# Kernel tuning notes

Measured on AMD Instinct MI355X. Metric: run time of the kernel, lower is better.

The kernel has to match this reference:

```python
import jax, jax.numpy as jnp
import numpy as np

D_MODEL = 2048
N_HEADS = 32
N_KV = 8
HEAD_DIM = D_MODEL // N_HEADS  # 64
D_FF = 8192
ROPE_BASE = 10000.0
EPS = 1e-5
B, S = 2, 2048


def setup_inputs() -> dict:
    key = jax.random.key(0)
    ks = jax.random.split(key, 8)
    s = 0.02
    qkv_out = (N_HEADS + 2 * N_KV) * HEAD_DIM
    return {
        "x": jax.random.normal(ks[0], (B, S, D_MODEL), jnp.float32),
        "w_norm1": jnp.ones((D_MODEL,), jnp.float32),
        "w_qkv": jax.random.normal(ks[1], (D_MODEL, qkv_out), jnp.float32) * s,
        "w_out": jax.random.normal(ks[2], (D_MODEL, D_MODEL), jnp.float32) * s,
        "w_norm2": jnp.ones((D_MODEL,), jnp.float32),
        "w_gate": jax.random.normal(ks[3], (D_MODEL, D_FF), jnp.float32) * s,
        "w_up": jax.random.normal(ks[4], (D_MODEL, D_FF), jnp.float32) * s,
        "w_down": jax.random.normal(ks[5], (D_FF, D_MODEL), jnp.float32) * s,
    }


def _rmsnorm(x, w):
    var = jnp.mean(x * x, axis=-1, keepdims=True)
    return x * jax.lax.rsqrt(var + EPS) * w


def _rope(x, cos, sin):
    # x: [b, s, h, d]; cos/sin: [s, d/2]; non-interleaved (NeoX half split)
    half = x.shape[-1] // 2
    x1, x2 = x[..., :half], x[..., half:]
    c = cos[None, :, None, :]
    sn = sin[None, :, None, :]
    return jnp.concatenate([x1 * c - x2 * sn, x1 * sn + x2 * c], axis=-1)


def _forward(x, w_norm1, w_qkv, w_out, w_norm2, w_gate, w_up, w_down):
    b, s, d = x.shape
    # --- attention block ---
    h = _rmsnorm(x, w_norm1)
    qkv = h @ w_qkv  # [b, s, (H + 2*KV) * hd]
    q = qkv[..., : N_HEADS * HEAD_DIM].reshape(b, s, N_HEADS, HEAD_DIM)
    kv = qkv[..., N_HEADS * HEAD_DIM:].reshape(b, s, 2, N_KV, HEAD_DIM)
    k, v = kv[:, :, 0], kv[:, :, 1]

    inv_freq = 1.0 / (ROPE_BASE ** (jnp.arange(0, HEAD_DIM, 2, dtype=jnp.float32) / HEAD_DIM))
    t = jnp.arange(s, dtype=jnp.float32)
    freqs = t[:, None] * inv_freq[None, :]  # [s, hd/2]
    cos, sin = jnp.cos(freqs), jnp.sin(freqs)
    q = _rope(q, cos, sin)
    k = _rope(k, cos, sin)

    # GQA: repeat_interleave kv heads to match q heads
    g = N_HEADS // N_KV
    k = jnp.repeat(k, g, axis=2)  # [b, s, H, hd]
    v = jnp.repeat(v, g, axis=2)

    scale = 1.0 / np.sqrt(HEAD_DIM)
    scores = jnp.einsum("bqhd,bkhd->bhqk", q, k) * scale
    causal = jnp.tril(jnp.ones((s, s), bool))
    scores = jnp.where(causal[None, None], scores, jnp.finfo(scores.dtype).min)
    attn = jax.nn.softmax(scores, axis=-1)
    ctx = jnp.einsum("bhqk,bkhd->bqhd", attn, v).reshape(b, s, N_HEADS * HEAD_DIM)
    x = x + ctx @ w_out

    # --- MLP block (SwiGLU) ---
    h2 = _rmsnorm(x, w_norm2)
    mlp = (jax.nn.silu(h2 @ w_gate) * (h2 @ w_up)) @ w_down
    return x + mlp


def reference(x, w_norm1, w_qkv, w_out, w_norm2, w_gate, w_up, w_down):
    return _forward(x, w_norm1, w_qkv, w_out, w_norm2, w_gate, w_up, w_down)
```

## Files before the change

kernel.cpp:

```cpp
#include <hip/hip_runtime.h>
#include <stdint.h>

#define D_MODEL 2048
#define S_LEN   2048
#define NTOK    4096
#define QKV_N   3072
#define DFF     8192

typedef float  f32x4   __attribute__((ext_vector_type(4)));
typedef float  f32x16  __attribute__((ext_vector_type(16)));
typedef __bf16 bf16x8  __attribute__((ext_vector_type(8)));
typedef unsigned short u16;
typedef unsigned short u16x8 __attribute__((ext_vector_type(8)));

__device__ __forceinline__ float b2f(u16 u){ union{float f; uint32_t i;} v; v.i = ((uint32_t)u) << 16; return v.f; }
__device__ __forceinline__ u16 f2b(float f){
  union{float f; uint32_t i;} v; v.f = f;
  uint32_t r = v.i + 0x7FFFu + ((v.i >> 16) & 1u);
  return (u16)(r >> 16);
}

__device__ __forceinline__ void gload_lds16(const void* gsrc, void* ldst){
  __builtin_amdgcn_global_load_lds(
      (const __attribute__((address_space(1))) void*)gsrc,
      (__attribute__((address_space(3))) void*)ldst,
      16, 0, 0);
}

__device__ __forceinline__ void conv_tiles(const float* W, u16* WT,
    int Nfull, int Kt, int Nt, int k0g, int n0g, void* ldsbuf)
{
  if (W == nullptr) return;
  float* tf = (float*)ldsbuf;
  const int tt  = threadIdx.x;
  const int nTn = Nt >> 6;
  const int nT  = (Kt >> 6) * nTn;
  const int bid = (blockIdx.z * gridDim.y + blockIdx.y) * gridDim.x + blockIdx.x;
  const int gsz = gridDim.x * gridDim.y * gridDim.z;
  const int c4 = (tt & 15) << 2;
  const int r  = tt >> 4;
  for (int tile = bid; tile < nT; tile += gsz) {
    const int k0 = (tile / nTn) << 6, n0 = (tile % nTn) << 6;
    __syncthreads();
    if (tt < 256) {
#pragma unroll
      for (int i = 0; i < 4; ++i) {
        int row = r + i * 16;
        float4 v = *reinterpret_cast<const float4*>(&W[(size_t)(k0g + k0 + row) * Nfull + n0g + n0 + c4]);
        tf[row * 65 + c4 + 0] = v.x; tf[row * 65 + c4 + 1] = v.y;
        tf[row * 65 + c4 + 2] = v.z; tf[row * 65 + c4 + 3] = v.w;
      }
    }
    __syncthreads();
    if (tt < 256) {
#pragma unroll
      for (int i = 0; i < 4; ++i) {
        int n = r + i * 16;
        ushort4 ov;
        ov.x = f2b(tf[(c4 + 0) * 65 + n]); ov.y = f2b(tf[(c4 + 1) * 65 + n]);
        ov.z = f2b(tf[(c4 + 2) * 65 + n]); ov.w = f2b(tf[(c4 + 3) * 65 + n]);
        *reinterpret_cast<ushort4*>(&WT[(size_t)(n0 + n) * Kt + k0 + c4]) = ov;
      }
    }
  }
}

__global__ __launch_bounds__(256) void wconv_kernel(const float* __restrict__ W, u16* __restrict__ WT,
                                                    int Nfull, int Kt, int Nt, int k0g, int n0g)
{
  __shared__ float tile[64 * 65];
  conv_tiles(W, WT, Nfull, Kt, Nt, k0g, n0g, tile);
}

__global__ void sincos_kernel(float* __restrict__ ct, float* __restrict__ st)
{
  int idx = blockIdx.x * 256 + threadIdx.x;
  if (idx >= S_LEN * 32) return;
  int p = idx >> 5, i = idx & 31;
  double freq = pow(10000.0, -((double)(2*i)) / 64.0);
  double ang  = (double)p * freq;
  ct[idx] = (float)cos(ang);
  st[idx] = (float)sin(ang);
}

template<bool BF16IN>
__global__ __launch_bounds__(256) void rmsnorm_kernel(const void* __restrict__ xin, const float* __restrict__ w, u16* __restrict__ out,
                                                      float* __restrict__ xout,
                                                      const float* cvW, u16* cvWT, int cvNfull, int cvKt, int cvNt, int cvK0g, int cvN0g)
{
  __shared__ float tfbuf[64 * 65];
  const int row = blockIdx.x;
  const int t = threadIdx.x;
  float v[8];
  if (BF16IN) {
    const u16* xr = ((const u16*)xin) + (size_t)row * D_MODEL;
    u16x8 a = *reinterpret_cast<const u16x8*>(&xr[t*8]);
#pragma unroll
    for (int j = 0; j < 8; ++j) v[j] = b2f(a[j]);
  } else {
    const float* xr = ((const float*)xin) + (size_t)row * D_MODEL;
    float4 a = *reinterpret_cast<const float4*>(&xr[t*8]);
    float4 c = *reinterpret_cast<const float4*>(&xr[t*8+4]);
    v[0]=a.x; v[1]=a.y; v[2]=a.z; v[3]=a.w; v[4]=c.x; v[5]=c.y; v[6]=c.z; v[7]=c.w;
  }
  if (xout) {
    float4 o0 = {v[0], v[1], v[2], v[3]};
    float4 o1 = {v[4], v[5], v[6], v[7]};
    *reinterpret_cast<float4*>(&xout[(size_t)row * D_MODEL + t*8])     = o0;
    *reinterpret_cast<float4*>(&xout[(size_t)row * D_MODEL + t*8 + 4]) = o1;
  }
  float ss = 0.f;
#pragma unroll
  for (int j = 0; j < 8; ++j) ss += v[j]*v[j];
#pragma unroll
  for (int d = 1; d < 64; d <<= 1) ss += __shfl_xor(ss, d);
  __shared__ float red[4];
  if ((t & 63) == 0) red[t >> 6] = ss;
  __syncthreads();
  ss = red[0] + red[1] + red[2] + red[3];
  const float sc = rsqrtf(ss * (1.0f / (float)D_MODEL) + 1e-5f);
  float4 w0 = *reinterpret_cast<const float4*>(&w[t*8]);
  float4 w1 = *reinterpret_cast<const float4*>(&w[t*8+4]);
  u16x8 o;
  o[0]=f2b(v[0]*sc*w0.x); o[1]=f2b(v[1]*sc*w0.y); o[2]=f2b(v[2]*sc*w0.z); o[3]=f2b(v[3]*sc*w0.w);
  o[4]=f2b(v[4]*sc*w1.x); o[5]=f2b(v[5]*sc*w1.y); o[6]=f2b(v[6]*sc*w1.z); o[7]=f2b(v[7]*sc*w1.w);
  *reinterpret_cast<u16x8*>(&out[(size_t)row * D_MODEL + t*8]) = o;
  conv_tiles(cvW, cvWT, cvNfull, cvKt, cvNt, cvK0g, cvN0g, tfbuf);
}

template<int EPI>
__device__ __forceinline__ void epi_store(size_t idx, float v, float* Cf, u16* Cb,
                                          const float* resf, const u16* resb, const u16* other)
{
  if (EPI == 2)      Cb[idx] = f2b(v / (1.0f + __expf(-v)));
  else if (EPI == 3) Cb[idx] = f2b(v * b2f(other[idx]));
  else if (EPI == 4) Cb[idx] = f2b(v);
  else if (EPI == 5) Cf[idx] += v;
  else if (EPI == 6) Cb[idx] = f2b(v + resf[idx]);
  else if (EPI == 7) Cf[idx] = v + b2f(resb[idx]);
  else if (EPI == 8) { if (blockIdx.z == 0) Cf[idx] += v; else Cb[idx] = f2b(v); }
}

template<int EPI>
__global__ __launch_bounds__(512, 2) void gemm8p_kernel(
    const u16* __restrict__ A, const u16* __restrict__ BT,
    int K, int lda, int ldb, int ldc, int n_off, int kstep,
    float* Cf, u16* Cb,
    const float* __restrict__ resf, const u16* __restrict__ resb, const u16* other,
    const float* cvW, u16* cvWT, int cvNfull, int cvKt, int cvNt, int cvK0g, int cvN0g)
{
  __shared__ u16 lds[65536];
  const int tid = threadIdx.x;
  const int w = tid >> 6, lane = tid & 63;
  const int g = lane >> 4, lr = lane & 15;
  const int wm = w >> 2, wn = w & 3;
  const int bn = blockIdx.x, bm = blockIdx.y;
  const int koff = blockIdx.z * kstep;
  const int NT = K >> 6;
  const int NI = NT >> 1;

  const int srow = tid >> 3;
  const int sg   = (tid & 7) ^ (srow & 7);
  const u16* Asrc = A  + (size_t)(bm * 256) * lda + koff;
  const u16* Bsrc = BT + (size_t)(bn * 256) * ldb + koff;

  const int agc0 = ((0 + g) ^ (lr & 7)) * 8;
  const int agc1 = ((4 + g) ^ (lr & 7)) * 8;

  f32x4 acc[8][4];
#pragma unroll
  for (int i = 0; i < 8; ++i)
#pragma unroll
    for (int j = 0; j < 4; ++j) acc[i][j] = (f32x4){0.f, 0.f, 0.f, 0.f};
  bf16x8 af[4][2], bf0[2][2], bf1[2][2];

#define STAGE_H(isB, h, b, T) do {                                           \
    int tc = ((T) < NT) ? (T) : (NT - 1);                                    \
    const u16* sb = (isB) ? Bsrc : Asrc;                                     \
    const int  sld = (isB) ? ldb : lda;                                      \
    const u16* s0 = sb + (size_t)((h)*128 + srow) * sld + tc*64 + sg*8;      \
    u16* dst = &lds[(b)*32768 + (isB)*16384 + (h)*8192 + tid*8];             \
    gload_lds16(s0, dst);                                                    \
    gload_lds16(s0 + (size_t)64 * sld, dst + 4096);                          \
  } while (0)

#define LOADA(mih, b) { _Pragma("unroll") for (int q = 0; q < 4; ++q) {      \
    const u16* rp = &lds[(b)*32768 + (wm*128 + (mih)*64 + q*16 + lr) * 64];  \
    af[q][0] = *(const bf16x8*)(rp + agc0);                                  \
    af[q][1] = *(const bf16x8*)(rp + agc1); } }

#define LOADB(dst, nih, b) { _Pragma("unroll") for (int nq = 0; nq < 2; ++nq) { \
    const u16* rp = &lds[(b)*32768 + 16384 + (wn*64 + (nih)*32 + nq*16 + lr) * 64]; \
    dst[nq][0] = *(const bf16x8*)(rp + agc0);                                \
    dst[nq][1] = *(const bf16x8*)(rp + agc1); } }

#define MM(mih, nih, BF) {                                                   \
    __builtin_amdgcn_s_setprio(1);                                           \
    _Pragma("unroll") for (int kk = 0; kk < 2; ++kk)                         \
      _Pragma("unroll") for (int q = 0; q < 4; ++q)                          \
        _Pragma("unroll") for (int nq = 0; nq < 2; ++nq)                     \
          acc[(mih)*4+q][(nih)*2+nq] = __builtin_amdgcn_mfma_f32_16x16x32_bf16( \
              af[q][kk], BF[nq][kk], acc[(mih)*4+q][(nih)*2+nq], 0, 0, 0);   \
    __builtin_amdgcn_s_setprio(0); }

#define SYNC_MID  __builtin_amdgcn_s_barrier();                              \
                  asm volatile("s_waitcnt lgkmcnt(0)" ::: "memory");         \
                  __builtin_amdgcn_sched_barrier(0);
#define PHEND     __builtin_amdgcn_s_barrier();
#define PHEND_VM  asm volatile("s_waitcnt vmcnt(4)" ::: "memory");           \
                  __builtin_amdgcn_s_barrier();

  STAGE_H(0, 0, 0, 0); STAGE_H(0, 1, 0, 0);
  STAGE_H(1, 0, 0, 0); STAGE_H(1, 1, 0, 0);
  STAGE_H(1, 0, 1, 1); STAGE_H(1, 1, 1, 1);
  asm volatile("s_waitcnt vmcnt(4)" ::: "memory");
  __builtin_amdgcn_s_barrier();

  for (int i = 0; i < NI; ++i) {
    const int t0 = 2 * i;
    LOADA(0, 0); LOADB(bf0, 0, 0);
    STAGE_H(0, 0, 1, t0 + 1);
    SYNC_MID; MM(0, 0, bf0); PHEND;
    LOADB(bf1, 1, 0);
    STAGE_H(0, 1, 1, t0 + 1);
    SYNC_MID; MM(0, 1, bf1); PHEND;
    LOADA(1, 0);
    STAGE_H(1, 0, 0, t0 + 2);
    SYNC_MID; MM(1, 1, bf1); PHEND;
    STAGE_H(1, 1, 0, t0 + 2);
    SYNC_MID; MM(1, 0, bf0); PHEND_VM;
    LOADA(0, 1); LOADB(bf0, 0, 1);
    STAGE_H(0, 0, 0, t0 + 2);
    SYNC_MID; MM(0, 0, bf0); PHEND;
    LOADB(bf1, 1, 1);
    STAGE_H(0, 1, 0, t0 + 2);
    SYNC_MID; MM(0, 1, bf1); PHEND;
    LOADA(1, 1);
    STAGE_H(1, 0, 1, t0 + 3);
    SYNC_MID; MM(1, 1, bf1); PHEND;
    STAGE_H(1, 1, 1, t0 + 3);
    SYNC_MID; MM(1, 0, bf0); PHEND_VM;
  }
#undef STAGE_H
#undef LOADA
#undef LOADB
#undef MM

#pragma unroll
  for (int mi = 0; mi < 8; ++mi) {
    const int rowOff = (mi >> 2) * 64 + (mi & 3) * 16;
#pragma unroll
    for (int ni = 0; ni < 4; ++ni) {
      const int colOff = (ni >> 1) * 32 + (ni & 1) * 16;
#pragma unroll
      for (int j = 0; j < 4; ++j) {
        int row = bm*256 + wm*128 + rowOff + g*4 + j;
        int col = n_off + bn*256 + wn*64 + colOff + lr;
        epi_store<EPI>((size_t)row * ldc + col, acc[mi][ni][j], Cf, Cb, resf, resb, other);
      }
    }
  }
  conv_tiles(cvW, cvWT, cvNfull, cvKt, cvNt, cvK0g, cvN0g, lds);
}

template<int EPI>
__global__ __launch_bounds__(512) void gemm128_kernel(
    const u16* __restrict__ A, const u16* __restrict__ BT,
    int K, int lda, int ldb, int ldc, int n_off,
    float* Cf, u16* Cb,
    const float* __restrict__ resf, const u16* __restrict__ resb, const u16* other,
    const float* cvW, u16* cvWT, int cvNfull, int cvKt, int cvNt, int cvK0g, int cvN0g)
{
  __shared__ u16 lds[49152];
  const int tid = threadIdx.x;
  const int w = tid >> 6, lane = tid & 63;
  const int g = lane >> 4, lr = lane & 15;
  const int wm = w >> 2, wn = w & 3;
  const int bn = blockIdx.x, bm = blockIdx.y;
  const int NT = K >> 6;
  const int NI = NT >> 1;

  const int srow = tid >> 3;
  const int sg   = (tid & 7) ^ (srow & 7);
  const u16* Asrc = A  + (size_t)(bm * 128) * lda;
  const u16* Bsrc = BT + (size_t)(bn * 256) * ldb;

  const int agc0 = ((0 + g) ^ (lr & 7)) * 8;
  const int agc1 = ((4 + g) ^ (lr & 7)) * 8;

  f32x4 acc[4][4];
#pragma unroll
  for (int i = 0; i < 4; ++i)
#pragma unroll
    for (int j = 0; j < 4; ++j) acc[i][j] = (f32x4){0.f, 0.f, 0.f, 0.f};
  bf16x8 af[2][2], bf0[2][2], bf1[2][2];

#define STAGE_A(b, T) do {                                                   \
    int tc = ((T) < NT) ? (T) : (NT - 1);                                    \
    const u16* s0 = Asrc + (size_t)srow * lda + tc*64 + sg*8;                \
    u16* dst = &lds[(b)*24576 + tid*8];                                      \
    gload_lds16(s0, dst);                                                    \
    gload_lds16(s0 + (size_t)64 * lda, dst + 4096);                          \
  } while (0)

#define STAGE_BH(h, b, T) do {                                               \
    int tc = ((T) < NT) ? (T) : (NT - 1);                                    \
    const u16* s0 = Bsrc + (size_t)((h)*128 + srow) * ldb + tc*64 + sg*8;    \
    u16* dst = &lds[(b)*24576 + 8192 + (h)*8192 + tid*8];                    \
    gload_lds16(s0, dst);                                                    \
    gload_lds16(s0 + (size_t)64 * ldb, dst + 4096);                         \
  } while (0)

#define LOADA(mih, b) { _Pragma("unroll") for (int q = 0; q < 2; ++q) {      \
    const u16* rp = &lds[(b)*24576 + (wm*64 + (mih)*32 + q*16 + lr) * 64];   \
    af[q][0] = *(const bf16x8*)(rp + agc0);                                  \
    af[q][1] = *(const bf16x8*)(rp + agc1); } }

#define LOADB(dst, nih, b) { _Pragma("unroll") for (int nq = 0; nq < 2; ++nq) { \
    const u16* rp = &lds[(b)*24576 + 8192 + (wn*64 + (nih)*32 + nq*16 + lr) * 64]; \
    dst[nq][0] = *(const bf16x8*)(rp + agc0);                                \
    dst[nq][1] = *(const bf16x8*)(rp + agc1); } }

#define MM(mih, nih, BF) {                                                   \
    __builtin_amdgcn_s_setprio(1);                                           \
    _Pragma("unroll") for (int kk = 0; kk < 2; ++kk)                         \
      _Pragma("unroll") for (int q = 0; q < 2; ++q)                          \
        _Pragma("unroll") for (int nq = 0; nq < 2; ++nq)                     \
          acc[(mih)*2+q][(nih)*2+nq] = __builtin_amdgcn_mfma_f32_16x16x32_bf16( \
              af[q][kk], BF[nq][kk], acc[(mih)*2+q][(nih)*2+nq], 0, 0, 0);   \
    __builtin_amdgcn_s_setprio(0); }

  STAGE_A(0, 0); STAGE_BH(0, 0, 0); STAGE_BH(1, 0, 0);
  STAGE_BH(0, 1, 1); STAGE_BH(1, 1, 1);
  asm volatile("s_waitcnt vmcnt(4)" ::: "memory");
  __builtin_amdgcn_s_barrier();

  for (int i = 0; i < NI; ++i) {
    const int t0 = 2 * i;
    LOADA(0, 0); LOADB(bf0, 0, 0);
    STAGE_A(1, t0 + 1);
    SYNC_MID; MM(0, 0, bf0); PHEND;
    LOADB(bf1, 1, 0);
    STAGE_BH(0, 0, t0 + 2);
    SYNC_MID; MM(0, 1, bf1); PHEND;
    LOADA(1, 0);
    STAGE_BH(1, 0, t0 + 2);
    SYNC_MID; MM(1, 1, bf1); PHEND;
    STAGE_A(0, t0 + 2);
    SYNC_MID; MM(1, 0, bf0);
    asm volatile("s_waitcnt vmcnt(6)" ::: "memory");
    __builtin_amdgcn_s_barrier();
    LOADA(0, 1); LOADB(bf0, 0, 1);
    SYNC_MID; MM(0, 0, bf0); PHEND;
    LOADB(bf1, 1, 1);
    STAGE_BH(0, 1, t0 + 3);
    SYNC_MID; MM(0, 1, bf1); PHEND;
    LOADA(1, 1);
    STAGE_BH(1, 1, t0 + 3);
    SYNC_MID; MM(1, 1, bf1); PHEND;
    SYNC_MID; MM(1, 0, bf0);
    asm volatile("s_waitcnt vmcnt(4)" ::: "memory");
    __builtin_amdgcn_s_barrier();
  }
#undef STAGE_A
#undef STAGE_BH
#undef LOADA
#undef LOADB
#undef MM
#undef SYNC_MID
#undef PHEND
#undef PHEND_VM

#pragma unroll
  for (int mi = 0; mi < 4; ++mi) {
    const int rowOff = (mi >> 1) * 32 + (mi & 1) * 16;
#pragma unroll
    for (int ni = 0; ni < 4; ++ni) {
      const int colOff = (ni >> 1) * 32 + (ni & 1) * 16;
#pragma unroll
      for (int j = 0; j < 4; ++j) {
        int row = bm*128 + wm*64 + rowOff + g*4 + j;
        int col = n_off + bn*256 + wn*64 + colOff + lr;
        epi_store<EPI>((size_t)row * ldc + col, acc[mi][ni][j], Cf, Cb, resf, resb, other);
      }
    }
  }
  conv_tiles(cvW, cvWT, cvNfull, cvKt, cvNt, cvK0g, cvN0g, lds);
}

__global__ __launch_bounds__(256) void rope_kernel(
    const u16* __restrict__ qkv, const float* __restrict__ ct, const float* __restrict__ st,
    u16* __restrict__ Kt, u16* __restrict__ VT)
{
  const int tok = blockIdx.x;
  const int b = tok >> 11, s = tok & (S_LEN - 1);
  const int w = threadIdx.x >> 6, lane = threadIdx.x & 63;
  const size_t base = (size_t)tok * QKV_N;
  for (int slot = w; slot < 16; slot += 4) {
    int col = (slot < 8) ? 2048 + slot * 64 : 2560 + (slot - 8) * 64;
    float v = b2f(qkv[base + col + lane]);
    if (slot < 8) {
      int i = lane & 31;
      float c = ct[s * 32 + i], sn = st[s * 32 + i];
      float p = b2f(qkv[base + col + (lane ^ 32)]);
      v = (lane < 32) ? (v * c - p * sn) : (v * c + p * sn);
    }
    u16 ob = f2b(v);
    if (slot < 8) Kt[((size_t)(b * 8 + slot)     * S_LEN + s) * 64 + lane] = ob;
    else          VT[((size_t)(b * 8 + slot - 8) * 64 + lane) * S_LEN + s] = ob;
  }
}

#define ASCALE 0.1803368801111204f
__global__ __launch_bounds__(256, 2) void attn_kernel(
    const u16* __restrict__ qkv, const u16* __restrict__ Kt,
    const u16* __restrict__ VT, u16* __restrict__ ctx,
    const float* __restrict__ ct, const float* __restrict__ st,
    const float* cvW, u16* cvWT, int cvNfull, int cvKt, int cvNt, int cvK0g, int cvN0g)
{
  __shared__ float tfbuf[64 * 65];
  const int bh  = blockIdx.x;
  const int y   = blockIdx.y;
  const int wid = threadIdx.x >> 6;
  const int lane = threadIdx.x & 63;
  const int b = bh >> 5, h = bh & 31;
  const int kvh = (b << 3) + (h >> 2);
  const int jj = y * 4 + wid;
  const int cq = lane & 31;
  const int hi = lane >> 5;

  const u16* Kp = Kt + (size_t)kvh * S_LEN * 64 + cq * 64 + hi * 8;
  const u16* Vbase = VT + (size_t)kvh * 64 * S_LEN + hi * 8;
  const u16* Vp[4];
#pragma unroll
  for (int v = 0; v < 4; ++v)
    Vp[v] = Vbase + (size_t)((v & 1) * 32 + cq) * S_LEN + (v >> 1) * 16;

  __shared__ float xch[4][32];

#define ATT_LOADK(KF, T) { _Pragma("unroll") for (int q_ = 0; q_ < 4; ++q_) \
    KF[q_] = *(const bf16x8*)(Kp + (T) * 2048 + q_ * 16); }
#define ATT_LOADV(VF, T) { _Pragma("unroll") for (int v_ = 0; v_ < 4; ++v_) \
    VF[v_] = *(const bf16x8*)(Vp[v_] + (T) * 32); }

#define ATT_QK(S, KF) do {                                                   \
    S = (f32x16){};                                                          \
    S = __builtin_amdgcn_mfma_f32_32x32x16_bf16(KF[0], qf[0], S, 0, 0, 0);   \
    S = __builtin_amdgcn_mfma_f32_32x32x16_bf16(KF[1], qf[1], S, 0, 0, 0);   \
    S = __builtin_amdgcn_mfma_f32_32x32x16_bf16(KF[2], qf[2], S, 0, 0, 0);   \
    S = __builtin_amdgcn_mfma_f32_32x32x16_bf16(KF[3], qf[3], S, 0, 0, 0);   \
  } while (0)

#define ATT_FIN(S, VF, T) do {                                               \
    float p[16];                                                             \
    _Pragma("unroll") for (int r = 0; r < 16; ++r) p[r] = S[r];              \
    if ((T) == nt - 1) {                                                     \
      _Pragma("unroll") for (int r = 0; r < 16; ++r) {                       \
        int kk = (r & 3) + 8 * (r >> 2) + 4 * hi;                            \
        if (kk > cq) p[r] = -1e30f;                                          \
      }                                                                      \
    }                                                                        \
    float m0_ = fmaxf(fmaxf(p[0], p[1]), p[2]);                              \
    float m1_ = fmaxf(fmaxf(p[3], p[4]), p[5]);                              \
    float m2_ = fmaxf(fmaxf(p[6], p[7]), p[8]);                              \
    float m3_ = fmaxf(fmaxf(p[9], p[10]), p[11]);                            \
    float m4_ = fmaxf(fmaxf(p[12], p[13]), p[14]);                           \
    float tmax = fmaxf(fmaxf(fmaxf(m0_, m1_), m2_), fmaxf(fmaxf(m3_, m4_), p[15])); \
    tmax = fmaxf(tmax, __shfl_xor(tmax, 32));                                \
    if (!__all(tmax <= m + 8.0f)) {                                          \
      float mn = fmaxf(m, tmax);                                             \
      float corr = exp2f(m - mn);                                            \
      m = mn;                                                                \
      l *= corr;                                                             \
      if (hi == 0) xch[wid][cq] = corr;                                      \
      asm volatile("s_waitcnt lgkmcnt(0)" ::: "memory");                     \
      __builtin_amdgcn_sched_barrier(0);                                     \
      float4 c0 = *reinterpret_cast<const float4*>(&xch[wid][4 * hi + 0]);   \
      float4 c1 = *reinterpret_cast<const float4*>(&xch[wid][4 * hi + 8]);   \
      float4 c2 = *reinterpret_cast<const float4*>(&xch[wid][4 * hi + 16]);  \
      float4 c3 = *reinterpret_cast<const float4*>(&xch[wid][4 * hi + 24]);  \
      float ca[16] = {c0.x,c0.y,c0.z,c0.w, c1.x,c1.y,c1.z,c1.w,              \
                      c2.x,c2.y,c2.z,c2.w, c3.x,c3.y,c3.z,c3.w};             \
      _Pragma("unroll") for (int r = 0; r < 16; ++r) { o0[r] *= ca[r]; o1[r] *= ca[r]; } \
    }                                                                        \
    _Pragma("unroll") for (int r = 0; r < 16; ++r) p[r] = exp2f(p[r] - m);   \
    {                                                                        \
      float a0 = p[0]+p[1], a1 = p[2]+p[3], a2 = p[4]+p[5], a3 = p[6]+p[7];  \
      float a4 = p[8]+p[9], a5 = p[10]+p[11], a6 = p[12]+p[13], a7 = p[14]+p[15]; \
      float b0_ = a0+a1, b1_ = a2+a3, b2_ = a4+a5, b3_ = a6+a7;              \
      l += (b0_+b1_) + (b2_+b3_);                                            \
    }                                                                        \
    uint32_t wds[8], pw[8];                                                  \
    _Pragma("unroll") for (int j = 0; j < 8; ++j) {                          \
      uint32_t wv;                                                           \
      asm("v_cvt_pk_bf16_f32 %0, %1, %2" : "=v"(wv) : "v"(p[2*j]), "v"(p[2*j+1])); \
      wds[j] = wv;                                                           \
    }                                                                        \
    _Pragma("unroll") for (int j = 0; j < 8; ++j) pw[j] = __shfl_xor(wds[j], 32); \
    union { uint32_t u[4]; bf16x8 v; } pa0, pa1;                             \
    pa0.u[0] = hi ? pw[2]  : wds[0];                                         \
    pa0.u[1] = hi ? pw[3]  : wds[1];                                         \
    pa0.u[2] = hi ? wds[2] : pw[0];                                          \
    pa0.u[3] = hi ? wds[3] : pw[1];                                          \
    pa1.u[0] = hi ? pw[6]  : wds[4];                                         \
    pa1.u[1] = hi ? pw[7]  : wds[5];                                         \
    pa1.u[2] = hi ? wds[6] : pw[4];                                          \
    pa1.u[3] = hi ? wds[7] : pw[5];                                          \
    o0 = __builtin_amdgcn_mfma_f32_32x32x16_bf16(pa0.v, VF[0], o0, 0, 0, 0); \
    o0 = __builtin_amdgcn_mfma_f32_32x32x16_bf16(pa1.v, VF[2], o0, 0, 0, 0); \
    o1 = __builtin_amdgcn_mfma_f32_32x32x16_bf16(pa0.v, VF[1], o1, 0, 0, 0); \
    o1 = __builtin_amdgcn_mfma_f32_32x32x16_bf16(pa1.v, VF[3], o1, 0, 0, 0); \
  } while (0)

#pragma unroll 1
  for (int task = 0; task < 2; ++task) {
    const int qt = task ? (63 - jj) : jj;
    const int q0 = qt << 5;
    const int nt = qt + 1;

    bf16x8 qf[4];
    {
      const u16* Qr = qkv + (size_t)(b * S_LEN + q0 + cq) * QKV_N + h * 64 + hi * 8;
      u16 qr[4][8];
#pragma unroll
      for (int t = 0; t < 4; ++t)
        *reinterpret_cast<u16x8*>(qr[t]) = *reinterpret_cast<const u16x8*>(Qr + t * 16);
      const float* cb = ct + (size_t)(q0 + cq) * 32 + hi * 8;
      const float* sb = st + (size_t)(q0 + cq) * 32 + hi * 8;
      union { u16 u[8]; bf16x8 v; } qo[4];
#pragma unroll
      for (int t = 0; t < 2; ++t) {
        float4 c0 = *reinterpret_cast<const float4*>(cb + 16 * t);
        float4 c1 = *reinterpret_cast<const float4*>(cb + 16 * t + 4);
        float4 s0 = *reinterpret_cast<const float4*>(sb + 16 * t);
        float4 s1 = *reinterpret_cast<const float4*>(sb + 16 * t + 4);
        float cc[8] = {c0.x,c0.y,c0.z,c0.w, c1.x,c1.y,c1.z,c1.w};
        float ssn[8] = {s0.x,s0.y,s0.z,s0.w, s1.x,s1.y,s1.z,s1.w};
#pragma unroll
        for (int i = 0; i < 8; ++i) {
          float lo = b2f(qr[t][i]), hif = b2f(qr[t + 2][i]);
          qo[t].u[i]     = f2b((lo * cc[i] - hif * ssn[i]) * ASCALE);
          qo[t + 2].u[i] = f2b((hif * cc[i] + lo * ssn[i]) * ASCALE);
        }
      }
#pragma unroll
      for (int t = 0; t < 4; ++t) qf[t] = qo[t].v;
    }

    f32x16 o0 = {}, o1 = {};
    float m = -1e30f, l = 0.f;

    bf16x8 kfE[4], kfO[4], vfE[4], vfO[4];
    f32x16 sE, sO;
    ATT_LOADK(kfE, 0); ATT_LOADV(vfE, 0);
    if (nt > 1) ATT_LOADK(kfO, 1);
    ATT_QK(sE, kfE);

    for (int t = 0; t < nt; ) {
      if (t + 2 < nt) ATT_LOADK(kfE, t + 2);
      if (t + 1 < nt) { ATT_LOADV(vfO, t + 1); ATT_QK(sO, kfO); }
      ATT_FIN(sE, vfE, t);
      ++t; if (t >= nt) break;
      if (t + 2 < nt) ATT_LOADK(kfO, t + 2);
      if (t + 1 < nt) { ATT_LOADV(vfE, t + 1); ATT_QK(sE, kfE); }
      ATT_FIN(sO, vfO, t);
      ++t;
    }

    l += __shfl_xor(l, 32);
    float linv = 1.0f / l;
    if (hi == 0) xch[wid][cq] = linv;
    asm volatile("s_waitcnt lgkmcnt(0)" ::: "memory");
    __builtin_amdgcn_sched_barrier(0);
    float4 n0 = *reinterpret_cast<const float4*>(&xch[wid][4 * hi + 0]);
    float4 n1 = *reinterpret_cast<const float4*>(&xch[wid][4 * hi + 8]);
    float4 n2 = *reinterpret_cast<const float4*>(&xch[wid][4 * hi + 16]);
    float4 n3 = *reinterpret_cast<const float4*>(&xch[wid][4 * hi + 24]);
    float na[16] = {n0.x,n0.y,n0.z,n0.w, n1.x,n1.y,n1.z,n1.w,
                    n2.x,n2.y,n2.z,n2.w, n3.x,n3.y,n3.z,n3.w};
#pragma unroll
    for (int r = 0; r < 16; ++r) {
      int row = (r & 3) + 8 * (r >> 2) + 4 * hi;
      size_t base = (size_t)(b * S_LEN + q0 + row) * D_MODEL + h * 64;
      ctx[base + cq]      = f2b(o0[r] * na[r]);
      ctx[base + 32 + cq] = f2b(o1[r] * na[r]);
    }
  }
#undef ATT_LOADK
#undef ATT_LOADV
#undef ATT_QK
#undef ATT_FIN

  conv_tiles(cvW, cvWT, cvNfull, cvKt, cvNt, cvK0g, cvN0g, tfbuf);
}

#define NOCV nullptr, nullptr, 0, 0, 0, 0, 0
extern "C" void kernel_launch(void* const* d_in, const int* in_sizes, int n_in,
                              void* d_out, int out_size, void* d_ws, size_t ws_size,
                              hipStream_t stream)
{
  const float* x     = (const float*)d_in[0];
  const float* wn1   = (const float*)d_in[1];
  const float* wqkv  = (const float*)d_in[2];
  const float* wout  = (const float*)d_in[3];
  const float* wn2   = (const float*)d_in[4];
  const float* wgate = (const float*)d_in[5];
  const float* wup   = (const float*)d_in[6];
  const float* wdown = (const float*)d_in[7];
  float* out = (float*)d_out;
  char* ws = (char*)d_ws;

  float* cosT  = (float*)(ws + 0);
  float* sinT  = (float*)(ws + 262144);
  u16*   slotA = (u16*)  (ws + 524288);
  u16*   slotB = (u16*)  (ws + 17301504);
  u16*   x1b   = (u16*)  (ws + 34078720);
  char*  S     = ws + 50855936;
  u16*   hB    = (u16*)(S + 0);
  u16*   qkvB  = (u16*)(S + 16777216);
  u16*   kB    = (u16*)(S + 41943040);
  u16*   vtB   = (u16*)(S + 46137344);
  u16*   ctxB  = (u16*)(S + 0);
  u16*   h2B   = (u16*)(S + 0);
  u16*   slab  = (u16*)(S + 16777216);

  sincos_kernel<<<dim3(256), 256, 0, stream>>>(cosT, sinT);
  rmsnorm_kernel<false><<<dim3(NTOK), 256, 0, stream>>>(x, wn1, hB, nullptr, NOCV);
  wconv_kernel<<<dim3(1536), 256, 0, stream>>>(wqkv, slotA, 3072, 2048, 3072, 0, 0);

  gemm128_kernel<4><<<dim3(12, 32), 512, 0, stream>>>(hB, slotA, 2048, 2048, 2048, 3072, 0,
      nullptr, qkvB, nullptr, nullptr, nullptr, wout, slotB, 2048, 2048, 2048, 0, 0);
  rope_kernel<<<dim3(NTOK), 256, 0, stream>>>(qkvB, cosT, sinT, kB, vtB);
  attn_kernel<<<dim3(64, 8), 256, 0, stream>>>(qkvB, kB, vtB, ctxB, cosT, sinT,
      wgate, slotA, 8192, 2048, 4096, 0, 0);

  gemm128_kernel<6><<<dim3(8, 32), 512, 0, stream>>>(ctxB, slotB, 2048, 2048, 2048, 2048, 0,
      nullptr, x1b, x, nullptr, nullptr, NOCV);

  rmsnorm_kernel<true><<<dim3(NTOK), 256, 0, stream>>>(x1b, wn2, h2B, nullptr,
      wup, slotB, 8192, 2048, 4096, 0, 0);

  gemm8p_kernel<2><<<dim3(16, 16), 512, 0, stream>>>(h2B, slotA, 2048, 2048, 2048, 4096, 0, 0,
      nullptr, slab, nullptr, nullptr, nullptr, NOCV);
  gemm8p_kernel<3><<<dim3(16, 16), 512, 0, stream>>>(h2B, slotB, 2048, 2048, 2048, 4096, 0, 0,
      nullptr, slab, nullptr, nullptr, slab, wdown, slotA, 2048, 4096, 2048, 0, 0);
  gemm128_kernel<7><<<dim3(8, 32), 512, 0, stream>>>(slab, slotA, 4096, 4096, 4096, 2048, 0,
      out, nullptr, nullptr, x1b, nullptr, wgate, slotB, 8192, 2048, 4096, 0, 4096);
  gemm8p_kernel<2><<<dim3(16, 16), 512, 0, stream>>>(h2B, slotB, 2048, 2048, 2048, 4096, 0, 0,
      nullptr, slab, nullptr, nullptr, nullptr, wup, slotA, 8192, 2048, 4096, 0, 4096);
  gemm8p_kernel<3><<<dim3(16, 16), 512, 0, stream>>>(h2B, slotA, 2048, 2048, 2048, 4096, 0, 0,
      nullptr, slab, nullptr, nullptr, slab, wdown, slotB, 2048, 4096, 2048, 4096, 0);
  gemm128_kernel<5><<<dim3(8, 32), 512, 0, stream>>>(slab, slotB, 4096, 4096, 4096, 2048, 0,
      out, nullptr, nullptr, nullptr, nullptr, NOCV);
}
```

Baseline: 792.0 us.

## Fuse gate and up GEMMs with interleaved weights and SwiGLU epilogue

Gate and up weight columns are interleaved during the bf16 conversion, so one GEMM computes both projections and applies SiLU(gate)*up in its epilogue through a lane shuffle. This replaces two GEMM launches per half (one of them rereading and rewriting the slab) with a single launch. It also adds an XCD-aware block-index swizzle to the GEMM kernels and reshuffles where the weight conversions are overlapped, now allowing two conversion jobs per GEMM. In exchange, half of the epilogue lanes store nothing, the output writes become strided, and workspace buffer reuse gets more intricate.

Result: faster. 772.8 us (-2.4%).

```diff
diff --git a/kernel.cpp b/kernel.cpp
--- a/kernel.cpp
+++ b/kernel.cpp
@@ -27,8 +27,8 @@
       16, 0, 0);
 }
 
-__device__ __forceinline__ void conv_tiles(const float* W, u16* WT,
-    int Nfull, int Kt, int Nt, int k0g, int n0g, void* ldsbuf)
+__device__ __forceinline__ void conv_tiles(const float* W, const float* W2, u16* WT,
+    int Nfull, int Kt, int Nt, int k0g, int n0g, int rmul, void* ldsbuf)
 {
   if (W == nullptr) return;
   float* tf = (float*)ldsbuf;
@@ -41,27 +41,31 @@
   const int r  = tt >> 4;
   for (int tile = bid; tile < nT; tile += gsz) {
     const int k0 = (tile / nTn) << 6, n0 = (tile % nTn) << 6;
-    __syncthreads();
-    if (tt < 256) {
-#pragma unroll
-      for (int i = 0; i < 4; ++i) {
-        int row = r + i * 16;
-        float4 v = *reinterpret_cast<const float4*>(&W[(size_t)(k0g + k0 + row) * Nfull + n0g + n0 + c4]);
-        tf[row * 65 + c4 + 0] = v.x; tf[row * 65 + c4 + 1] = v.y;
-        tf[row * 65 + c4 + 2] = v.z; tf[row * 65 + c4 + 3] = v.w;
+    for (int m = 0; m < 2; ++m) {
+      const float* Ws = m ? W2 : W;
+      if (m && W2 == nullptr) break;
+      __syncthreads();
+      if (tt < 256) {
+#pragma unroll
+        for (int i = 0; i < 4; ++i) {
+          int row = r + i * 16;
+          float4 v = *reinterpret_cast<const float4*>(&Ws[(size_t)(k0g + k0 + row) * Nfull + n0g + n0 + c4]);
+          tf[row * 65 + c4 + 0] = v.x; tf[row * 65 + c4 + 1] = v.y;
+          tf[row * 65 + c4 + 2] = v.z; tf[row * 65 + c4 + 3] = v.w;
+        }
+      }
+      __syncthreads();
+      if (tt < 256) {
+#pragma unroll
+        for (int i = 0; i < 4; ++i) {
+          int n = r + i * 16;
+          ushort4 ov;
+          ov.x = f2b(tf[(c4 + 0) * 65 + n]); ov.y = f2b(tf[(c4 + 1) * 65 + n]);
+          ov.z = f2b(tf[(c4 + 2) * 65 + n]); ov.w = f2b(tf[(c4 + 3) * 65 + n]);
+          *reinterpret_cast<ushort4*>(&WT[(size_t)((n0 + n) * rmul + m) * Kt + k0 + c4]) = ov;
+        }
       }
     }
-    __syncthreads();
-    if (tt < 256) {
-#pragma unroll
-      for (int i = 0; i < 4; ++i) {
-        int n = r + i * 16;
-        ushort4 ov;
-        ov.x = f2b(tf[(c4 + 0) * 65 + n]); ov.y = f2b(tf[(c4 + 1) * 65 + n]);
-        ov.z = f2b(tf[(c4 + 2) * 65 + n]); ov.w = f2b(tf[(c4 + 3) * 65 + n]);
-        *reinterpret_cast<ushort4*>(&WT[(size_t)(n0 + n) * Kt + k0 + c4]) = ov;
-      }
-    }
   }
 }
 
@@ -69,7 +73,7 @@
                                                     int Nfull, int Kt, int Nt, int k0g, int n0g)
 {
   __shared__ float tile[64 * 65];
-  conv_tiles(W, WT, Nfull, Kt, Nt, k0g, n0g, tile);
+  conv_tiles(W, nullptr, WT, Nfull, Kt, Nt, k0g, n0g, 1, tile);
 }
 
 __global__ void sincos_kernel(float* __restrict__ ct, float* __restrict__ st)
@@ -85,8 +89,7 @@
 
 template<bool BF16IN>
 __global__ __launch_bounds__(256) void rmsnorm_kernel(const void* __restrict__ xin, const float* __restrict__ w, u16* __restrict__ out,
-                                                      float* __restrict__ xout,
-                                                      const float* cvW, u16* cvWT, int cvNfull, int cvKt, int cvNt, int cvK0g, int cvN0g)
+                                                      const float* cvW, const float* cvW2, u16* cvWT, int cvNfull, int cvKt, int cvNt, int cvK0g, int cvN0g, int cvRm)
 {
   __shared__ float tfbuf[64 * 65];
   const int row = blockIdx.x;
@@ -102,12 +105,6 @@
     float4 a = *reinterpret_cast<const float4*>(&xr[t*8]);
     float4 c = *reinterpret_cast<const float4*>(&xr[t*8+4]);
     v[0]=a.x; v[1]=a.y; v[2]=a.z; v[3]=a.w; v[4]=c.x; v[5]=c.y; v[6]=c.z; v[7]=c.w;
-  }
-  if (xout) {
-    float4 o0 = {v[0], v[1], v[2], v[3]};
-    float4 o1 = {v[4], v[5], v[6], v[7]};
-    *reinterpret_cast<float4*>(&xout[(size_t)row * D_MODEL + t*8])     = o0;
-    *reinterpret_cast<float4*>(&xout[(size_t)row * D_MODEL + t*8 + 4]) = o1;
   }
   float ss = 0.f;
 #pragma unroll
@@ -125,7 +122,7 @@
   o[0]=f2b(v[0]*sc*w0.x); o[1]=f2b(v[1]*sc*w0.y); o[2]=f2b(v[2]*sc*w0.z); o[3]=f2b(v[3]*sc*w0.w);
   o[4]=f2b(v[4]*sc*w1.x); o[5]=f2b(v[5]*sc*w1.y); o[6]=f2b(v[6]*sc*w1.z); o[7]=f2b(v[7]*sc*w1.w);
   *reinterpret_cast<u16x8*>(&out[(size_t)row * D_MODEL + t*8]) = o;
-  conv_tiles(cvW, cvWT, cvNfull, cvKt, cvNt, cvK0g, cvN0g, tfbuf);
+  conv_tiles(cvW, cvW2, cvWT, cvNfull, cvKt, cvNt, cvK0g, cvN0g, cvRm, tfbuf);
 }
 
 template<int EPI>
@@ -138,31 +135,41 @@
   else if (EPI == 5) Cf[idx] += v;
   else if (EPI == 6) Cb[idx] = f2b(v + resf[idx]);
   else if (EPI == 7) Cf[idx] = v + b2f(resb[idx]);
-  else if (EPI == 8) { if (blockIdx.z == 0) Cf[idx] += v; else Cb[idx] = f2b(v); }
+  else if (EPI == 9) {
+    float pv = __shfl_xor(v, 1);
+    float gate = (threadIdx.x & 1) ? pv : v;
+    float up   = (threadIdx.x & 1) ? v  : pv;
+    if (!(threadIdx.x & 1)) Cb[idx] = f2b(gate / (1.0f + __expf(-gate)) * up);
+  }
 }
 
 template<int EPI>
 __global__ __launch_bounds__(512, 2) void gemm8p_kernel(
-    const u16* __restrict__ A, const u16* __restrict__ BT,
-    int K, int lda, int ldb, int ldc, int n_off, int kstep,
+    const u16* __restrict__ A, const u16* __restrict__ BT, const u16* __restrict__ BT2,
+    int K, int lda, int ldb, int ldc, int n_off,
     float* Cf, u16* Cb,
     const float* __restrict__ resf, const u16* __restrict__ resb, const u16* other,
-    const float* cvW, u16* cvWT, int cvNfull, int cvKt, int cvNt, int cvK0g, int cvN0g)
+    const float* cvW, const float* cvW2, u16* cvWT, int cvNfull, int cvKt, int cvNt, int cvK0g, int cvN0g, int cvRm)
 {
   __shared__ u16 lds[65536];
   const int tid = threadIdx.x;
   const int w = tid >> 6, lane = tid & 63;
   const int g = lane >> 4, lr = lane & 15;
   const int wm = w >> 2, wn = w & 3;
-  const int bn = blockIdx.x, bm = blockIdx.y;
-  const int koff = blockIdx.z * kstep;
+  int fid = blockIdx.y * gridDim.x + blockIdx.x;
+  const int nwg = gridDim.x * gridDim.y;
+  fid = (fid & 7) * (nwg >> 3) + (fid >> 3);
+  const int bn = fid % gridDim.x, bm = fid / gridDim.x;
   const int NT = K >> 6;
   const int NI = NT >> 1;
 
   const int srow = tid >> 3;
   const int sg   = (tid & 7) ^ (srow & 7);
-  const u16* Asrc = A  + (size_t)(bm * 256) * lda + koff;
-  const u16* Bsrc = BT + (size_t)(bn * 256) * ldb + koff;
+  const u16* Asrc = A + (size_t)(bm * 256) * lda;
+  const u16* Bsrc;
+  if (EPI == 9) Bsrc = (bn < 16) ? BT + (size_t)(bn * 256) * ldb
+                                 : BT2 + (size_t)(bn * 256 - 4096) * ldb;
+  else          Bsrc = BT + (size_t)(bn * 256) * ldb;
 
   const int agc0 = ((0 + g) ^ (lr & 7)) * 8;
   const int agc1 = ((4 + g) ^ (lr & 7)) * 8;
@@ -256,11 +263,13 @@
       for (int j = 0; j < 4; ++j) {
         int row = bm*256 + wm*128 + rowOff + g*4 + j;
         int col = n_off + bn*256 + wn*64 + colOff + lr;
-        epi_store<EPI>((size_t)row * ldc + col, acc[mi][ni][j], Cf, Cb, resf, resb, other);
+        size_t idx = (EPI == 9) ? ((size_t)row * ldc + (col >> 1))
+                                : ((size_t)row * ldc + col);
+        epi_store<EPI>(idx, acc[mi][ni][j], Cf, Cb, resf, resb, other);
       }
     }
   }
-  conv_tiles(cvW, cvWT, cvNfull, cvKt, cvNt, cvK0g, cvN0g, lds);
+  conv_tiles(cvW, cvW2, cvWT, cvNfull, cvKt, cvNt, cvK0g, cvN0g, cvRm, lds);
 }
 
 template<int EPI>
@@ -269,14 +278,18 @@
     int K, int lda, int ldb, int ldc, int n_off,
     float* Cf, u16* Cb,
     const float* __restrict__ resf, const u16* __restrict__ resb, const u16* other,
-    const float* cvW, u16* cvWT, int cvNfull, int cvKt, int cvNt, int cvK0g, int cvN0g)
+    const float* c1W, const float* c1W2, u16* c1WT, int c1Nfull, int c1Kt, int c1Nt, int c1K0g, int c1N0g, int c1Rm,
+    const float* c2W, const float* c2W2, u16* c2WT, int c2Nfull, int c2Kt, int c2Nt, int c2K0g, int c2N0g, int c2Rm)
 {
   __shared__ u16 lds[49152];
   const int tid = threadIdx.x;
   const int w = tid >> 6, lane = tid & 63;
   const int g = lane >> 4, lr = lane & 15;
   const int wm = w >> 2, wn = w & 3;
-  const int bn = blockIdx.x, bm = blockIdx.y;
+  int fid = blockIdx.y * gridDim.x + blockIdx.x;
+  const int nwg = gridDim.x * gridDim.y;
+  fid = (fid & 7) * (nwg >> 3) + (fid >> 3);
+  const int bn = fid % gridDim.x, bm = fid / gridDim.x;
   const int NT = K >> 6;
   const int NI = NT >> 1;
 
@@ -385,7 +398,8 @@
       }
     }
   }
-  conv_tiles(cvW, cvWT, cvNfull, cvKt, cvNt, cvK0g, cvN0g, lds);
+  conv_tiles(c1W, c1W2, c1WT, c1Nfull, c1Kt, c1Nt, c1K0g, c1N0g, c1Rm, lds);
+  conv_tiles(c2W, c2W2, c2WT, c2Nfull, c2Kt, c2Nt, c2K0g, c2N0g, c2Rm, lds);
 }
 
 __global__ __launch_bounds__(256) void rope_kernel(
@@ -416,7 +430,7 @@
     const u16* __restrict__ qkv, const u16* __restrict__ Kt,
     const u16* __restrict__ VT, u16* __restrict__ ctx,
     const float* __restrict__ ct, const float* __restrict__ st,
-    const float* cvW, u16* cvWT, int cvNfull, int cvKt, int cvNt, int cvK0g, int cvN0g)
+    const float* cvW, const float* cvW2, u16* cvWT, int cvNfull, int cvKt, int cvNt, int cvK0g, int cvN0g, int cvRm)
 {
   __shared__ float tfbuf[64 * 65];
   const int bh  = blockIdx.x;
@@ -591,10 +605,10 @@
 #undef ATT_QK
 #undef ATT_FIN
 
-  conv_tiles(cvW, cvWT, cvNfull, cvKt, cvNt, cvK0g, cvN0g, tfbuf);
-}
-
-#define NOCV nullptr, nullptr, 0, 0, 0, 0, 0
+  conv_tiles(cvW, cvW2, cvWT, cvNfull, cvKt, cvNt, cvK0g, cvN0g, cvRm, tfbuf);
+}
+
+#define NOCV nullptr, nullptr, nullptr, 0, 0, 0, 0, 0, 1
 extern "C" void kernel_launch(void* const* d_in, const int* in_sizes, int n_in,
                               void* d_out, int out_size, void* d_ws, size_t ws_size,
                               hipStream_t stream)
@@ -610,46 +624,48 @@
   float* out = (float*)d_out;
   char* ws = (char*)d_ws;
 
-  float* cosT  = (float*)(ws + 0);
-  float* sinT  = (float*)(ws + 262144);
-  u16*   slotA = (u16*)  (ws + 524288);
-  u16*   slotB = (u16*)  (ws + 17301504);
-  u16*   x1b   = (u16*)  (ws + 34078720);
-  char*  S     = ws + 50855936;
-  u16*   hB    = (u16*)(S + 0);
-  u16*   qkvB  = (u16*)(S + 16777216);
-  u16*   kB    = (u16*)(S + 41943040);
-  u16*   vtB   = (u16*)(S + 46137344);
-  u16*   ctxB  = (u16*)(S + 0);
-  u16*   h2B   = (u16*)(S + 0);
-  u16*   slab  = (u16*)(S + 16777216);
+  float* cosT = (float*)(ws + 0);
+  float* sinT = (float*)(ws + 262144);
+  u16*   U1   = (u16*)  (ws + 524288);
+  u16*   U2   = (u16*)  (ws + 17301504);
+  u16*   x1b  = (u16*)  (ws + 34078720);
+  char*  S    = ws + 50855936;
+  u16*   hB   = (u16*)(S + 0);
+  u16*   qkvB = (u16*)(S + 16777216);
+  u16*   kB   = (u16*)(S + 41943040);
+  u16*   vtB  = (u16*)(S + 46137344);
+  u16*   ctxB = (u16*)(S + 0);
+  u16*   h2B  = (u16*)(S + 0);
+  u16*   slab = (u16*)(S + 16777216);
+  u16*   U7   = (u16*)(S + 50331648);
 
   sincos_kernel<<<dim3(256), 256, 0, stream>>>(cosT, sinT);
-  rmsnorm_kernel<false><<<dim3(NTOK), 256, 0, stream>>>(x, wn1, hB, nullptr, NOCV);
-  wconv_kernel<<<dim3(1536), 256, 0, stream>>>(wqkv, slotA, 3072, 2048, 3072, 0, 0);
-
-  gemm128_kernel<4><<<dim3(12, 32), 512, 0, stream>>>(hB, slotA, 2048, 2048, 2048, 3072, 0,
-      nullptr, qkvB, nullptr, nullptr, nullptr, wout, slotB, 2048, 2048, 2048, 0, 0);
+  rmsnorm_kernel<false><<<dim3(NTOK), 256, 0, stream>>>(x, wn1, hB, NOCV);
+  wconv_kernel<<<dim3(1536), 256, 0, stream>>>(wqkv, U1, 3072, 2048, 3072, 0, 0);
+
+  gemm128_kernel<4><<<dim3(12, 32), 512, 0, stream>>>(hB, U1, 2048, 2048, 2048, 3072, 0,
+      nullptr, qkvB, nullptr, nullptr, nullptr,
+      wout, nullptr, U7, 2048, 2048, 2048, 0, 0, 1, NOCV);
   rope_kernel<<<dim3(NTOK), 256, 0, stream>>>(qkvB, cosT, sinT, kB, vtB);
   attn_kernel<<<dim3(64, 8), 256, 0, stream>>>(qkvB, kB, vtB, ctxB, cosT, sinT,
-      wgate, slotA, 8192, 2048, 4096, 0, 0);
-
-  gemm128_kernel<6><<<dim3(8, 32), 512, 0, stream>>>(ctxB, slotB, 2048, 2048, 2048, 2048, 0,
-      nullptr, x1b, x, nullptr, nullptr, NOCV);
-
-  rmsnorm_kernel<true><<<dim3(NTOK), 256, 0, stream>>>(x1b, wn2, h2B, nullptr,
-      wup, slotB, 8192, 2048, 4096, 0, 0);
-
-  gemm8p_kernel<2><<<dim3(16, 16), 512, 0, stream>>>(h2B, slotA, 2048, 2048, 2048, 4096, 0, 0,
+      wgate, wup, U1, 8192, 2048, 2048, 0, 0, 2);
+
+  gemm128_kernel<6><<<dim3(8, 32), 512, 0, stream>>>(ctxB, U7, 2048, 2048, 2048, 2048, 0,
+      nullptr, x1b, x, nullptr, nullptr,
+      wgate, wup, U2, 8192, 2048, 2048, 0, 2048, 2, NOCV);
+
+  rmsnorm_kernel<true><<<dim3(NTOK), 256, 0, stream>>>(x1b, wn2, h2B,
+      wdown, nullptr, U7, 2048, 4096, 2048, 0, 0, 1);
+
+  gemm8p_kernel<9><<<dim3(32, 16), 512, 0, stream>>>(h2B, U1, U2, 2048, 2048, 2048, 4096, 0,
       nullptr, slab, nullptr, nullptr, nullptr, NOCV);
-  gemm8p_kernel<3><<<dim3(16, 16), 512, 0, stream>>>(h2B, slotB, 2048, 2048, 2048, 4096, 0, 0,
-      nullptr, slab, nullptr, nullptr, slab, wdown, slotA, 2048, 4096, 2048, 0, 0);
-  gemm128_kernel<7><<<dim3(8, 32), 512, 0, stream>>>(slab, slotA, 4096, 4096, 4096, 2048, 0,
-      out, nullptr, nullptr, x1b, nullptr, wgate, slotB, 8192, 2048, 4096, 0, 4096);
-  gemm8p_kernel<2><<<dim3(16, 16), 512, 0, stream>>>(h2B, slotB, 2048, 2048, 2048, 4096, 0, 0,
-      nullptr, slab, nullptr, nullptr, nullptr, wup, slotA, 8192, 2048, 4096, 0, 4096);
-  gemm8p_kernel<3><<<dim3(16, 16), 512, 0, stream>>>(h2B, slotA, 2048, 2048, 2048, 4096, 0, 0,
-      nullptr, slab, nullptr, nullptr, slab, wdown, slotB, 2048, 4096, 2048, 4096, 0);
-  gemm128_kernel<5><<<dim3(8, 32), 512, 0, stream>>>(slab, slotB, 4096, 4096, 4096, 2048, 0,
-      out, nullptr, nullptr, nullptr, nullptr, NOCV);
-}
+  gemm128_kernel<7><<<dim3(8, 32), 512, 0, stream>>>(slab, U7, 4096, 4096, 4096, 2048, 0,
+      out, nullptr, nullptr, x1b, nullptr,
+      wgate, wup, U1, 8192, 2048, 2048, 0, 4096, 2,
+      wgate, wup, U2, 8192, 2048, 2048, 0, 6144, 2);
+  gemm8p_kernel<9><<<dim3(32, 16), 512, 0, stream>>>(h2B, U1, U2, 2048, 2048, 2048, 4096, 0,
+      nullptr, slab, nullptr, nullptr, nullptr,
+      wdown, nullptr, U7, 2048, 4096, 2048, 4096, 0, 1);
+  gemm128_kernel<5><<<dim3(8, 32), 512, 0, stream>>>(slab, U7, 4096, 4096, 4096, 2048, 0,
+      out, nullptr, nullptr, nullptr, nullptr, NOCV, NOCV);
+}
```
